# Optimization experiments

Hardware: AMD Instinct MI355X
Metric: run time of the kernel (lower is better)

The kernel has to match this reference:

```python
import jax, jax.numpy as jnp
import numpy as np

H = 128          # hidden_size
EF = 2           # expansion_factor
E = H * EF       # expanded hidden size
K = 4            # conv kernel size
R = 8            # dt_rank = ceil(128/16)
L = 2            # num_layers
BATCH = 2
SEQ = 1024
EPS = 1e-5


def rmsnorm(x, w):
    return x * jax.lax.rsqrt(jnp.mean(x * x, axis=-1, keepdims=True) + EPS) * w


def causal_conv1d(x, w, b):
    # x: (b, l, E); w: (E, 1, K) depthwise; left-pad K-1 => causal, output len l
    xt = jnp.transpose(x, (0, 2, 1))  # (b, E, l)
    out = jax.lax.conv_general_dilated(
        xt, w, window_strides=(1,), padding=[(K - 1, 0)],
        dimension_numbers=("NCH", "OIH", "NCH"), feature_group_count=E)
    out = out + b[None, :, None]
    return jnp.transpose(out, (0, 2, 1))


def sscan(xc, delta, A, Bm, Cm, Dp):
    # xc, delta: (b,l,E); A: (E,n); Bm, Cm: (b,l,n); Dp: (E,)
    deltaA = jnp.exp(jnp.einsum('bld,dn->bldn', delta, A))          # (b,l,E,n)
    deltaBx = jnp.einsum('bld,bln,bld->bldn', delta, Bm, xc)        # (b,l,E,n)

    def step(h, inp):
        dA_t, dBx_t, C_t = inp           # (b,E,n), (b,E,n), (b,n)
        h = dA_t * h + dBx_t
        y = jnp.einsum('bdn,bn->bd', h, C_t)
        return h, y

    b = xc.shape[0]
    h0 = jnp.zeros((b, E, A.shape[1]), dtype=xc.dtype)
    _, ys = jax.lax.scan(
        step, h0,
        (jnp.transpose(deltaA, (1, 0, 2, 3)),
         jnp.transpose(deltaBx, (1, 0, 2, 3)),
         jnp.transpose(Cm, (1, 0, 2))))
    y = jnp.transpose(ys, (1, 0, 2))     # (b,l,E)
    return y + Dp * xc


def mamba_block(x, in_w, in_b, out_w, out_b, pl_w, pl_b, dt_w, dt_b,
                conv_w, conv_b, A_log, Dp):
    xz = x @ in_w + in_b                 # (b,l,2E)
    xc, skip = jnp.split(xz, [E], axis=-1)
    xc = jax.nn.silu(causal_conv1d(xc, conv_w, conv_b))
    # ssm
    A = -jnp.exp(A_log)                  # (E,H)
    dbc = xc @ pl_w + pl_b               # (b,l,R+2H)
    delta, Bm, Cm = jnp.split(dbc, [R, R + H], axis=-1)
    delta = jax.nn.softplus(delta @ dt_w + dt_b)   # (b,l,E)
    y = sscan(xc, delta, A, Bm, Cm, Dp)
    y = y * jax.nn.silu(skip)
    return y @ out_w + out_b


def forward(x, in_w, in_b, out_w, out_b, pl_w, pl_b, dt_w, dt_b,
            conv_w, conv_b, A_log, Dp, norm_w, final_norm_w):
    for i in range(L):
        x = mamba_block(rmsnorm(x, norm_w[i]), in_w[i], in_b[i], out_w[i],
                        out_b[i], pl_w[i], pl_b[i], dt_w[i], dt_b[i],
                        conv_w[i], conv_b[i], A_log[i], Dp[i]) + x
    return rmsnorm(x, final_norm_w)


def setup_inputs() -> dict:
    key = jax.random.key(0)
    ks = jax.random.split(key, 12)
    s = 0.02
    x = jax.random.normal(ks[0], (BATCH, SEQ, H), dtype=jnp.float32)
    in_w = jax.random.normal(ks[1], (L, H, 2 * E)) * s
    in_b = jnp.zeros((L, 2 * E))
    out_w = jax.random.normal(ks[2], (L, E, H)) * s
    out_b = jnp.zeros((L, H))
    pl_w = jax.random.normal(ks[3], (L, E, R + 2 * H)) * s
    pl_b = jnp.zeros((L, R + 2 * H))
    dt_w = jax.random.normal(ks[4], (L, R, E)) * s
    dt_b = jnp.zeros((L, E))
    conv_w = jax.random.normal(ks[5], (L, E, 1, K)) * (1.0 / np.sqrt(K))
    conv_b = jnp.zeros((L, E))
    A_log = jnp.broadcast_to(jnp.log(jnp.arange(1, H + 1, dtype=jnp.float32)),
                             (L, E, H))
    Dp = jnp.ones((L, E))
    norm_w = jnp.ones((L, H))
    final_norm_w = jnp.ones((H,))
    return {"x": x, "in_w": in_w, "in_b": in_b, "out_w": out_w,
            "out_b": out_b, "pl_w": pl_w, "pl_b": pl_b, "dt_w": dt_w,
            "dt_b": dt_b, "conv_w": conv_w, "conv_b": conv_b,
            "A_log": A_log, "Dp": Dp, "norm_w": norm_w,
            "final_norm_w": final_norm_w}


def reference(x, in_w, in_b, out_w, out_b, pl_w, pl_b, dt_w, dt_b,
              conv_w, conv_b, A_log, Dp, norm_w, final_norm_w):
    return forward(x, in_w, in_b, out_w, out_b, pl_w, pl_b, dt_w, dt_b,
                   conv_w, conv_b, A_log, Dp, norm_w, final_norm_w)
```

## Files before the change

### kernel.cpp

```cpp
#include <hip/hip_runtime.h>
#include <hip/hip_bf16.h>

#define HH 128
#define EE 256
#define KK 4
#define RR 8
#define LL 2
#define BB 2
#define SS 1024
#define BT (BB*SS)
#define NJ (RR+2*HH)
#define GG 16
#define CH (SS/GG)
#define EPS 1e-5f
#define LOG2E 1.44269504088896f

__device__ __forceinline__ float silu_f(float v) {
    return v / (1.0f + __expf(-v));
}

__global__ __launch_bounds__(512) void k_norm_inproj(
    const float* __restrict__ xres, const float* __restrict__ inw,
    const float* __restrict__ inb, const float* __restrict__ nw,
    float* __restrict__ xz)
{
    __shared__ float xn[16][128];
    const int bt0 = blockIdx.x * 16;
    const int tid = threadIdx.x;
    {
        const int t = tid >> 5, g = tid & 31;
        const float4 xv = *(const float4*)(xres + (bt0 + t) * HH + g * 4);
        float ss = xv.x*xv.x + xv.y*xv.y + xv.z*xv.z + xv.w*xv.w;
        #pragma unroll
        for (int m = 16; m >= 1; m >>= 1) ss += __shfl_xor(ss, m);
        const float rs = rsqrtf(ss * (1.0f / HH) + EPS);
        const float4 wv = *(const float4*)(nw + g * 4);
        float4 o;
        o.x = xv.x * rs * wv.x; o.y = xv.y * rs * wv.y;
        o.z = xv.z * rs * wv.z; o.w = xv.w * rs * wv.w;
        *(float4*)(&xn[t][g * 4]) = o;
    }
    __syncthreads();
    const int j = tid;
    float acc[16];
    const float bj = inb[j];
    #pragma unroll
    for (int t = 0; t < 16; t++) acc[t] = bj;
    float w0n = inw[0*512 + j], w1n = inw[1*512 + j];
    float w2n = inw[2*512 + j], w3n = inw[3*512 + j];
    for (int k4 = 0; k4 < 32; k4++) {
        const float w0 = w0n, w1 = w1n, w2 = w2n, w3 = w3n;
        if (k4 < 31) {
            const int k = (k4 + 1) * 4;
            w0n = inw[(k+0)*512 + j]; w1n = inw[(k+1)*512 + j];
            w2n = inw[(k+2)*512 + j]; w3n = inw[(k+3)*512 + j];
        }
        const int k = k4 * 4;
        #pragma unroll
        for (int t = 0; t < 16; t++) {
            const float4 xv = *(const float4*)(&xn[t][k]);
            acc[t] += w0*xv.x + w1*xv.y + w2*xv.z + w3*xv.w;
        }
    }
    #pragma unroll
    for (int t = 0; t < 16; t++) xz[(bt0 + t) * 512 + j] = acc[t];
}

__global__ __launch_bounds__(256) void k_conv(
    const float* __restrict__ xz, const float* __restrict__ cw,
    const float* __restrict__ cb, float* __restrict__ xcT)
{
    const int e = threadIdx.x;
    const int tile = blockIdx.x;
    const int b = tile >> 6;
    const int t0 = (tile & 63) * 16;
    const float w0 = cw[e*4+0], w1 = cw[e*4+1], w2 = cw[e*4+2], w3 = cw[e*4+3];
    const float bias = cb[e];
    const float* xp = xz + (size_t)(b * SS) * 512 + e;
    float xm3 = (t0 >= 3) ? xp[(t0-3)*512] : 0.0f;
    float xm2 = (t0 >= 2) ? xp[(t0-2)*512] : 0.0f;
    float xm1 = (t0 >= 1) ? xp[(t0-1)*512] : 0.0f;
    float* orow = xcT + (size_t)e * BT + b * SS + t0;
    for (int jq = 0; jq < 4; jq++) {
        const int t = t0 + jq * 4;
        float4 ob; float v;
        const float x0 = xp[(t+0)*512];
        v = bias + w3*x0 + w2*xm1 + w1*xm2 + w0*xm3; ob.x = silu_f(v);
        const float x1 = xp[(t+1)*512];
        v = bias + w3*x1 + w2*x0 + w1*xm1 + w0*xm2;  ob.y = silu_f(v);
        const float x2 = xp[(t+2)*512];
        v = bias + w3*x2 + w2*x1 + w1*x0 + w0*xm1;   ob.z = silu_f(v);
        const float x3 = xp[(t+3)*512];
        v = bias + w3*x3 + w2*x2 + w1*x1 + w0*x0;    ob.w = silu_f(v);
        *(float4*)(orow + jq * 4) = ob;
        xm3 = x1; xm2 = x2; xm1 = x3;
    }
}

__global__ __launch_bounds__(320) void k_plproj(
    const float* __restrict__ xcT, const float* __restrict__ plw,
    const float* __restrict__ plb, float* __restrict__ dbcT)
{
    __shared__ float xs[8][256];
    const int bt0 = blockIdx.x * 8;
    const int tid = threadIdx.x;
    if (tid < 256) {
        const int e = tid;
        const float* p = xcT + (size_t)e * BT + bt0;
        const float4 a = *(const float4*)(p);
        const float4 c = *(const float4*)(p + 4);
        xs[0][e] = a.x; xs[1][e] = a.y; xs[2][e] = a.z; xs[3][e] = a.w;
        xs[4][e] = c.x; xs[5][e] = c.y; xs[6][e] = c.z; xs[7][e] = c.w;
    }
    __syncthreads();
    if (tid >= NJ) return;
    const int j = tid;
    float acc[8];
    const float bj = plb[j];
    #pragma unroll
    for (int t = 0; t < 8; t++) acc[t] = bj;
    float w0n = plw[0*NJ + j], w1n = plw[1*NJ + j];
    float w2n = plw[2*NJ + j], w3n = plw[3*NJ + j];
    for (int e4 = 0; e4 < 64; e4++) {
        const float w0 = w0n, w1 = w1n, w2 = w2n, w3 = w3n;
        if (e4 < 63) {
            const int e = (e4 + 1) * 4;
            w0n = plw[(e+0)*NJ + j]; w1n = plw[(e+1)*NJ + j];
            w2n = plw[(e+2)*NJ + j]; w3n = plw[(e+3)*NJ + j];
        }
        const int e = e4 * 4;
        #pragma unroll
        for (int t = 0; t < 8; t++) {
            const float4 xv = *(const float4*)(&xs[t][e]);
            acc[t] += w0*xv.x + w1*xv.y + w2*xv.z + w3*xv.w;
        }
    }
    float* orow = dbcT + (size_t)j * BT + bt0;
    *(float4*)(orow)     = make_float4(acc[0], acc[1], acc[2], acc[3]);
    *(float4*)(orow + 4) = make_float4(acc[4], acc[5], acc[6], acc[7]);
}

__global__ __launch_bounds__(256) void k_delta(
    const float* __restrict__ dbcT, const float* __restrict__ dtw,
    const float* __restrict__ dtb, const float* __restrict__ xcT,
    float* __restrict__ deltaT, float* __restrict__ sT)
{
    const int e = blockIdx.x >> 3;
    const int bt = (blockIdx.x & 7) * 256 + threadIdx.x;
    float d = dtb[e];
    #pragma unroll
    for (int r = 0; r < RR; r++) d += dtw[r*EE + e] * dbcT[(size_t)r * BT + bt];
    float sp;
    if (d > 15.0f) sp = d;
    else sp = log1pf(__expf(d));
    const float xc = xcT[(size_t)e * BT + bt];
    deltaT[(size_t)e * BT + bt] = sp;
    sT[(size_t)e * BT + bt] = sp * xc;
}

__global__ __launch_bounds__(128, 3) void k_scan_local(
    const float* __restrict__ dbcT, const float* __restrict__ deltaT,
    const float* __restrict__ sT, const float* __restrict__ Alog,
    float* __restrict__ yT, float* __restrict__ hchain,
    float* __restrict__ dsum)
{
    __shared__ float part[4][16][68];
    __shared__ float ybuf[4][CH];
    const int blk = blockIdx.x;
    const int wgid = (blk & 7) * 256 + (blk >> 3);
    const int eq = wgid & 63;
    const int r0 = wgid >> 6;
    const int b = r0 >> 4;
    const int g = r0 & 15;
    const int e0 = eq * 4;
    const int n = threadIdx.x;
    const int t0 = g * CH;

    float An[4], h[4], cum[4];
    #pragma unroll
    for (int ee = 0; ee < 4; ee++) {
        An[ee] = -__expf(Alog[(e0 + ee) * HH + n]) * LOG2E;
        h[ee] = 0.0f; cum[ee] = 0.0f;
    }
    const float* Brow = dbcT + (size_t)(RR + n) * BT + b * SS + t0;
    const float* Crow = dbcT + (size_t)(RR + HH + n) * BT + b * SS + t0;
    const float* dr[4]; const float* sr[4];
    #pragma unroll
    for (int ee = 0; ee < 4; ee++) {
        dr[ee] = deltaT + (size_t)(e0 + ee) * BT + b * SS + t0;
        sr[ee] = sT + (size_t)(e0 + ee) * BT + b * SS + t0;
    }
    float4 pB = *(const float4*)Brow;
    float4 pC = *(const float4*)Crow;
    float4 pd[4], ps[4];
    #pragma unroll
    for (int ee = 0; ee < 4; ee++) {
        pd[ee] = *(const float4*)dr[ee];
        ps[ee] = *(const float4*)sr[ee];
    }
    const int tl = n >> 3, jj = n & 7;
    for (int sc = 0; sc < 4; sc++) {
        #pragma unroll
        for (int q = 0; q < 4; q++) {
            const int qq = sc * 4 + q;
            const float4 cB = pB, cC = pC;
            float4 cd[4], cs[4];
            #pragma unroll
            for (int ee = 0; ee < 4; ee++) { cd[ee] = pd[ee]; cs[ee] = ps[ee]; }
            if (qq < 15) {
                const int t = (qq + 1) * 4;
                pB = *(const float4*)(Brow + t);
                pC = *(const float4*)(Crow + t);
                #pragma unroll
                for (int ee = 0; ee < 4; ee++) {
                    pd[ee] = *(const float4*)(dr[ee] + t);
                    ps[ee] = *(const float4*)(sr[ee] + t);
                }
            }
            #pragma unroll
            for (int ee = 0; ee < 4; ee++) {
                float a;
                a = exp2f(cd[ee].x * An[ee]); h[ee] = a*h[ee] + cs[ee].x*cB.x;
                part[ee][q*4+0][n] = h[ee] * cC.x;
                a = exp2f(cd[ee].y * An[ee]); h[ee] = a*h[ee] + cs[ee].y*cB.y;
                part[ee][q*4+1][n] = h[ee] * cC.y;
                a = exp2f(cd[ee].z * An[ee]); h[ee] = a*h[ee] + cs[ee].z*cB.z;
                part[ee][q*4+2][n] = h[ee] * cC.z;
                a = exp2f(cd[ee].w * An[ee]); h[ee] = a*h[ee] + cs[ee].w*cB.w;
                part[ee][q*4+3][n] = h[ee] * cC.w;
                cum[ee] += (cd[ee].x + cd[ee].y) + (cd[ee].z + cd[ee].w);
            }
        }
        __syncthreads();
        #pragma unroll
        for (int ee = 0; ee < 4; ee++) {
            float s0 = 0, s1 = 0, s2 = 0, s3 = 0;
            #pragma unroll
            for (int i = 0; i < 4; i++) {
                const float4 p = *(const float4*)(&part[ee][tl][jj*16 + i*4]);
                s0 += p.x; s1 += p.y; s2 += p.z; s3 += p.w;
            }
            float r = (s0 + s1) + (s2 + s3);
            r += __shfl_xor(r, 1); r += __shfl_xor(r, 2); r += __shfl_xor(r, 4);
            if (jj == 0) ybuf[ee][sc*16 + tl] = r;
        }
        __syncthreads();
    }
    {
        const int ee = n >> 5, tt = n & 31;
        float* yp = yT + (size_t)(e0 + ee) * BT + b * SS + t0;
        yp[tt] = ybuf[ee][tt];
        yp[tt + 32] = ybuf[ee][tt + 32];
    }
    #pragma unroll
    for (int ee = 0; ee < 4; ee++)
        hchain[(size_t)(((b * EE + e0 + ee) * GG) + g) * 128 + n] = h[ee];
    if (n == 0) {
        #pragma unroll
        for (int ee = 0; ee < 4; ee++)
            dsum[(b * EE + e0 + ee) * GG + g] = cum[ee];
    }
}

__global__ __launch_bounds__(128) void k_scan_combine(
    const float* __restrict__ Alog, const float* __restrict__ dsum,
    float* __restrict__ hchain)
{
    const int be = blockIdx.x;
    const int e = be & 255;
    const int n = threadIdx.x;
    const float An = -__expf(Alog[e * HH + n]) * LOG2E;
    float h = 0.0f;
    for (int g = 0; g < GG; g++) {
        float* p = hchain + (size_t)(be * GG + g) * 128 + n;
        const float he = *p;
        *p = h;
        const float ds = dsum[be * GG + g];
        h = exp2f(An * ds) * h + he;
    }
}

__global__ __launch_bounds__(128, 3) void k_scan_fix(
    const float* __restrict__ dbcT, const float* __restrict__ deltaT,
    const float* __restrict__ Alog, const float* __restrict__ hchain,
    float* __restrict__ yT)
{
    __shared__ float part[4][16][68];
    __shared__ float ybuf[4][CH];
    const int blk = blockIdx.x;
    const int wgid = (blk & 7) * 240 + (blk >> 3);
    const int eq = wgid & 63;
    const int r0 = wgid >> 6;
    const int b = r0 / 15;
    const int g = 1 + (r0 % 15);
    const int e0 = eq * 4;
    const int n = threadIdx.x;
    const int t0 = g * CH;

    float An[4], w[4], D[4];
    #pragma unroll
    for (int ee = 0; ee < 4; ee++) {
        An[ee] = -__expf(Alog[(e0 + ee) * HH + n]) * LOG2E;
        w[ee] = hchain[(size_t)(((b * EE + e0 + ee) * GG) + g) * 128 + n];
        D[ee] = 0.0f;
    }
    const float* Crow = dbcT + (size_t)(RR + HH + n) * BT + b * SS + t0;
    const float* dr[4];
    #pragma unroll
    for (int ee = 0; ee < 4; ee++)
        dr[ee] = deltaT + (size_t)(e0 + ee) * BT + b * SS + t0;

    float4 pC = *(const float4*)Crow;
    float4 pd[4];
    #pragma unroll
    for (int ee = 0; ee < 4; ee++) pd[ee] = *(const float4*)dr[ee];

    const int tl = n >> 3, jj = n & 7;
    for (int sc = 0; sc < 4; sc++) {
        #pragma unroll
        for (int q = 0; q < 4; q++) {
            const int qq = sc * 4 + q;
            const float4 cC = pC;
            float4 cd[4];
            #pragma unroll
            for (int ee = 0; ee < 4; ee++) cd[ee] = pd[ee];
            if (qq < 15) {
                const int t = (qq + 1) * 4;
                pC = *(const float4*)(Crow + t);
                #pragma unroll
                for (int ee = 0; ee < 4; ee++)
                    pd[ee] = *(const float4*)(dr[ee] + t);
            }
            #pragma unroll
            for (int ee = 0; ee < 4; ee++) {
                D[ee] += cd[ee].x; part[ee][q*4+0][n] = exp2f(An[ee]*D[ee]) * w[ee] * cC.x;
                D[ee] += cd[ee].y; part[ee][q*4+1][n] = exp2f(An[ee]*D[ee]) * w[ee] * cC.y;
                D[ee] += cd[ee].z; part[ee][q*4+2][n] = exp2f(An[ee]*D[ee]) * w[ee] * cC.z;
                D[ee] += cd[ee].w; part[ee][q*4+3][n] = exp2f(An[ee]*D[ee]) * w[ee] * cC.w;
            }
        }
        __syncthreads();
        #pragma unroll
        for (int ee = 0; ee < 4; ee++) {
            float s0 = 0, s1 = 0, s2 = 0, s3 = 0;
            #pragma unroll
            for (int i = 0; i < 4; i++) {
                const float4 p = *(const float4*)(&part[ee][tl][jj*16 + i*4]);
                s0 += p.x; s1 += p.y; s2 += p.z; s3 += p.w;
            }
            float r = (s0 + s1) + (s2 + s3);
            r += __shfl_xor(r, 1); r += __shfl_xor(r, 2); r += __shfl_xor(r, 4);
            if (jj == 0) ybuf[ee][sc*16 + tl] = r;
        }
        __syncthreads();
    }
    {
        const int ee = n >> 5, tt = n & 31;
        float* yp = yT + (size_t)(e0 + ee) * BT + b * SS + t0;
        yp[tt] += ybuf[ee][tt];
        yp[tt + 32] += ybuf[ee][tt + 32];
    }
}

__global__ __launch_bounds__(256) void k_gate_outproj(
    const float* __restrict__ yT, const float* __restrict__ xcT,
    const float* __restrict__ xz, const float* __restrict__ Dp,
    const float* __restrict__ ow, const float* __restrict__ ob,
    float* __restrict__ xres)
{
    __shared__ float gs[16][256];
    __shared__ float part2[16][128];
    const int bt0 = blockIdx.x * 16;
    const int tid = threadIdx.x;
    {
        const int e = tid;
        const float dp = Dp[e];
        const float* yp = yT + (size_t)e * BT + bt0;
        const float* xp = xcT + (size_t)e * BT + bt0;
        #pragma unroll
        for (int tq = 0; tq < 4; tq++) {
            const float4 y4 = *(const float4*)(yp + tq * 4);
            const float4 x4 = *(const float4*)(xp + tq * 4);
            float sk;
            sk = xz[(size_t)(bt0 + tq*4 + 0) * 512 + 256 + e];
            gs[tq*4+0][e] = (y4.x + dp * x4.x) * silu_f(sk);
            sk = xz[(size_t)(bt0 + tq*4 + 1) * 512 + 256 + e];
            gs[tq*4+1][e] = (y4.y + dp * x4.y) * silu_f(sk);
            sk = xz[(size_t)(bt0 + tq*4 + 2) * 512 + 256 + e];
            gs[tq*4+2][e] = (y4.z + dp * x4.z) * silu_f(sk);
            sk = xz[(size_t)(bt0 + tq*4 + 3) * 512 + 256 + e];
            gs[tq*4+3][e] = (y4.w + dp * x4.w) * silu_f(sk);
        }
    }
    __syncthreads();
    const int j = tid & 127;
    const int kh = tid >> 7;
    float acc[16];
    #pragma unroll
    for (int t = 0; t < 16; t++) acc[t] = 0.0f;
    const int eb = kh * 128;
    float w0n = ow[(eb+0)*HH + j], w1n = ow[(eb+1)*HH + j];
    float w2n = ow[(eb+2)*HH + j], w3n = ow[(eb+3)*HH + j];
    for (int e4 = 0; e4 < 32; e4++) {
        const float w0 = w0n, w1 = w1n, w2 = w2n, w3 = w3n;
        if (e4 < 31) {
            const int e = eb + (e4 + 1) * 4;
            w0n = ow[(e+0)*HH + j]; w1n = ow[(e+1)*HH + j];
            w2n = ow[(e+2)*HH + j]; w3n = ow[(e+3)*HH + j];
        }
        const int e = eb + e4 * 4;
        #pragma unroll
        for (int t = 0; t < 16; t++) {
            const float4 g4 = *(const float4*)(&gs[t][e]);
            acc[t] += w0*g4.x + w1*g4.y + w2*g4.z + w3*g4.w;
        }
    }
    if (kh == 1) {
        #pragma unroll
        for (int t = 0; t < 16; t++) part2[t][j] = acc[t];
    }
    __syncthreads();
    if (kh == 0) {
        const float bj = ob[j];
        #pragma unroll
        for (int t = 0; t < 16; t++) {
            const float r = acc[t] + part2[t][j] + bj
                          + xres[(size_t)(bt0 + t) * HH + j];
            xres[(size_t)(bt0 + t) * HH + j] = r;
        }
    }
}

__global__ __launch_bounds__(64) void k_finalnorm(
    const float* __restrict__ xres, const float* __restrict__ fw,
    float* __restrict__ out)
{
    const int bt = blockIdx.x;
    const int tid = threadIdx.x;
    const float2 v = *(const float2*)(xres + (size_t)bt * HH + tid * 2);
    float ss = v.x*v.x + v.y*v.y;
    #pragma unroll
    for (int m = 32; m >= 1; m >>= 1) ss += __shfl_xor(ss, m);
    const float rs = rsqrtf(ss * (1.0f / HH) + EPS);
    const float2 w = *(const float2*)(fw + tid * 2);
    float2 o; o.x = v.x * rs * w.x; o.y = v.y * rs * w.y;
    *(float2*)(out + (size_t)bt * HH + tid * 2) = o;
}

extern "C" void kernel_launch(void* const* d_in, const int* in_sizes, int n_in,
                              void* d_out, int out_size, void* d_ws, size_t ws_size,
                              hipStream_t stream)
{
    const float* x      = (const float*)d_in[0];
    const float* in_w   = (const float*)d_in[1];
    const float* in_b   = (const float*)d_in[2];
    const float* out_w  = (const float*)d_in[3];
    const float* out_b  = (const float*)d_in[4];
    const float* pl_w   = (const float*)d_in[5];
    const float* pl_b   = (const float*)d_in[6];
    const float* dt_w   = (const float*)d_in[7];
    const float* dt_b   = (const float*)d_in[8];
    const float* conv_w = (const float*)d_in[9];
    const float* conv_b = (const float*)d_in[10];
    const float* A_log  = (const float*)d_in[11];
    const float* Dp     = (const float*)d_in[12];
    const float* norm_w = (const float*)d_in[13];
    const float* fnw    = (const float*)d_in[14];

    float* ws     = (float*)d_ws;
    float* xres   = ws;
    float* xz     = xres   + 262144;
    float* xcT    = xz     + 1048576;
    float* dbcT   = xcT    + 524288;
    float* deltaT = dbcT   + 540672;
    float* sT     = deltaT + 524288;
    float* yT     = sT     + 524288;
    float* hchain = yT     + 524288;
    float* dsum   = hchain + 1048576;

    hipMemcpyAsync(xres, x, (size_t)262144 * sizeof(float),
                   hipMemcpyDeviceToDevice, stream);

    for (int l = 0; l < LL; l++) {
        k_norm_inproj<<<BT/16, 512, 0, stream>>>(
            xres, in_w + (size_t)l*HH*2*EE, in_b + (size_t)l*2*EE,
            norm_w + (size_t)l*HH, xz);
        k_conv<<<128, 256, 0, stream>>>(
            xz, conv_w + (size_t)l*EE*KK, conv_b + (size_t)l*EE, xcT);
        k_plproj<<<BT/8, 320, 0, stream>>>(
            xcT, pl_w + (size_t)l*EE*NJ, pl_b + (size_t)l*NJ, dbcT);
        k_delta<<<EE*8, 256, 0, stream>>>(
            dbcT, dt_w + (size_t)l*RR*EE, dt_b + (size_t)l*EE, xcT, deltaT, sT);
        k_scan_local<<<BB*GG*(EE/4), 128, 0, stream>>>(
            dbcT, deltaT, sT, A_log + (size_t)l*EE*HH, yT, hchain, dsum);
        k_scan_combine<<<BB*EE, 128, 0, stream>>>(
            A_log + (size_t)l*EE*HH, dsum, hchain);
        k_scan_fix<<<BB*(GG-1)*(EE/4), 128, 0, stream>>>(
            dbcT, deltaT, A_log + (size_t)l*EE*HH, hchain, yT);
        k_gate_outproj<<<BT/16, 256, 0, stream>>>(
            yT, xcT, xz, Dp + (size_t)l*EE,
            out_w + (size_t)l*EE*HH, out_b + (size_t)l*HH, xres);
    }
    k_finalnorm<<<BT, 64, 0, stream>>>(xres, fnw, (float*)d_out);
}
```

Before: 283.6 us.

## Interleave B/C into time-major layout, halve channels per scan block, move dsum to delta

The projection kernel now writes B and C into an interleaved layout with four timesteps grouped per state index, so each scan thread reads B and C for four steps with contiguous float4 loads. The chunk delta sums move into k_delta as a wave-level shuffle reduction, which removes the cumulative-sum work from the scan. The scan local and fix kernels now handle 2 channels per block instead of 4, doubling the grid and raising the occupancy hint to 4 blocks per CU. The intent is more parallelism and fewer registers per thread, at the cost of reloading B and C once per 2 channels instead of once per 4.

```diff
diff --git a/kernel.cpp b/kernel.cpp
--- a/kernel.cpp
+++ b/kernel.cpp
@@ -99,7 +99,8 @@
 
 __global__ __launch_bounds__(320) void k_plproj(
     const float* __restrict__ xcT, const float* __restrict__ plw,
-    const float* __restrict__ plb, float* __restrict__ dbcT)
+    const float* __restrict__ plb, float* __restrict__ dtrows,
+    float* __restrict__ BC4)
 {
     __shared__ float xs[8][256];
     const int bt0 = blockIdx.x * 8;
@@ -135,105 +136,107 @@
             acc[t] += w0*xv.x + w1*xv.y + w2*xv.z + w3*xv.w;
         }
     }
-    float* orow = dbcT + (size_t)j * BT + bt0;
-    *(float4*)(orow)     = make_float4(acc[0], acc[1], acc[2], acc[3]);
-    *(float4*)(orow + 4) = make_float4(acc[4], acc[5], acc[6], acc[7]);
+    if (j < RR) {
+        float* orow = dtrows + (size_t)j * BT + bt0;
+        *(float4*)(orow)     = make_float4(acc[0], acc[1], acc[2], acc[3]);
+        *(float4*)(orow + 4) = make_float4(acc[4], acc[5], acc[6], acc[7]);
+    } else {
+        const int isC = (j >= RR + HH);
+        const int nn = isC ? (j - RR - HH) : (j - RR);
+        const int tq0 = bt0 >> 2;
+        float* p0 = BC4 + ((size_t)tq0 * 128 + nn) * 8 + (isC ? 4 : 0);
+        *(float4*)p0 = make_float4(acc[0], acc[1], acc[2], acc[3]);
+        float* p1 = BC4 + ((size_t)(tq0 + 1) * 128 + nn) * 8 + (isC ? 4 : 0);
+        *(float4*)p1 = make_float4(acc[4], acc[5], acc[6], acc[7]);
+    }
 }
 
 __global__ __launch_bounds__(256) void k_delta(
-    const float* __restrict__ dbcT, const float* __restrict__ dtw,
+    const float* __restrict__ dtrows, const float* __restrict__ dtw,
     const float* __restrict__ dtb, const float* __restrict__ xcT,
-    float* __restrict__ deltaT, float* __restrict__ sT)
+    float* __restrict__ deltaT, float* __restrict__ sT,
+    float* __restrict__ dsum)
 {
     const int e = blockIdx.x >> 3;
     const int bt = (blockIdx.x & 7) * 256 + threadIdx.x;
     float d = dtb[e];
     #pragma unroll
-    for (int r = 0; r < RR; r++) d += dtw[r*EE + e] * dbcT[(size_t)r * BT + bt];
+    for (int r = 0; r < RR; r++) d += dtw[r*EE + e] * dtrows[(size_t)r * BT + bt];
     float sp;
     if (d > 15.0f) sp = d;
     else sp = log1pf(__expf(d));
     const float xc = xcT[(size_t)e * BT + bt];
     deltaT[(size_t)e * BT + bt] = sp;
     sT[(size_t)e * BT + bt] = sp * xc;
-}
-
-__global__ __launch_bounds__(128, 3) void k_scan_local(
-    const float* __restrict__ dbcT, const float* __restrict__ deltaT,
+    float cs = sp;
+    #pragma unroll
+    for (int m = 1; m <= 32; m <<= 1) cs += __shfl_xor(cs, m);
+    if ((threadIdx.x & 63) == 0) {
+        const int b = bt >> 10;
+        const int g = (bt & 1023) >> 6;
+        dsum[(b * EE + e) * GG + g] = cs;
+    }
+}
+
+__global__ __launch_bounds__(128, 4) void k_scan_local(
+    const float* __restrict__ BC4, const float* __restrict__ deltaT,
     const float* __restrict__ sT, const float* __restrict__ Alog,
-    float* __restrict__ yT, float* __restrict__ hchain,
-    float* __restrict__ dsum)
-{
-    __shared__ float part[4][16][68];
-    __shared__ float ybuf[4][CH];
+    float* __restrict__ yT, float* __restrict__ hchain)
+{
+    __shared__ float part[2][16][68];
+    __shared__ float ybuf[2][CH];
     const int blk = blockIdx.x;
-    const int wgid = (blk & 7) * 256 + (blk >> 3);
-    const int eq = wgid & 63;
-    const int r0 = wgid >> 6;
+    const int wgid = (blk & 7) * 512 + (blk >> 3);
+    const int eq = wgid & 127;
+    const int r0 = wgid >> 7;
     const int b = r0 >> 4;
     const int g = r0 & 15;
-    const int e0 = eq * 4;
+    const int e0 = eq * 2;
     const int n = threadIdx.x;
     const int t0 = g * CH;
 
-    float An[4], h[4], cum[4];
-    #pragma unroll
-    for (int ee = 0; ee < 4; ee++) {
-        An[ee] = -__expf(Alog[(e0 + ee) * HH + n]) * LOG2E;
-        h[ee] = 0.0f; cum[ee] = 0.0f;
-    }
-    const float* Brow = dbcT + (size_t)(RR + n) * BT + b * SS + t0;
-    const float* Crow = dbcT + (size_t)(RR + HH + n) * BT + b * SS + t0;
-    const float* dr[4]; const float* sr[4];
-    #pragma unroll
-    for (int ee = 0; ee < 4; ee++) {
-        dr[ee] = deltaT + (size_t)(e0 + ee) * BT + b * SS + t0;
-        sr[ee] = sT + (size_t)(e0 + ee) * BT + b * SS + t0;
-    }
-    float4 pB = *(const float4*)Brow;
-    float4 pC = *(const float4*)Crow;
-    float4 pd[4], ps[4];
-    #pragma unroll
-    for (int ee = 0; ee < 4; ee++) {
-        pd[ee] = *(const float4*)dr[ee];
-        ps[ee] = *(const float4*)sr[ee];
-    }
+    float An0 = -__expf(Alog[(e0+0) * HH + n]) * LOG2E;
+    float An1 = -__expf(Alog[(e0+1) * HH + n]) * LOG2E;
+    float h0 = 0.0f, h1 = 0.0f;
+    const float* bc = BC4 + ((size_t)((b * 256 + g * 16) * 128 + n)) * 8;
+    const float* dr0 = deltaT + (size_t)(e0+0) * BT + b * SS + t0;
+    const float* dr1 = deltaT + (size_t)(e0+1) * BT + b * SS + t0;
+    const float* sr0 = sT + (size_t)(e0+0) * BT + b * SS + t0;
+    const float* sr1 = sT + (size_t)(e0+1) * BT + b * SS + t0;
+
+    float4 pB = *(const float4*)(bc);
+    float4 pC = *(const float4*)(bc + 4);
+    float4 pd0 = *(const float4*)dr0, pd1 = *(const float4*)dr1;
+    float4 ps0 = *(const float4*)sr0, ps1 = *(const float4*)sr1;
+
     const int tl = n >> 3, jj = n & 7;
     for (int sc = 0; sc < 4; sc++) {
         #pragma unroll
         for (int q = 0; q < 4; q++) {
             const int qq = sc * 4 + q;
             const float4 cB = pB, cC = pC;
-            float4 cd[4], cs[4];
-            #pragma unroll
-            for (int ee = 0; ee < 4; ee++) { cd[ee] = pd[ee]; cs[ee] = ps[ee]; }
+            const float4 cd0 = pd0, cd1 = pd1, cs0 = ps0, cs1 = ps1;
             if (qq < 15) {
+                const size_t off = (size_t)(qq + 1) * 1024;
+                pB = *(const float4*)(bc + off);
+                pC = *(const float4*)(bc + off + 4);
                 const int t = (qq + 1) * 4;
-                pB = *(const float4*)(Brow + t);
-                pC = *(const float4*)(Crow + t);
-                #pragma unroll
-                for (int ee = 0; ee < 4; ee++) {
-                    pd[ee] = *(const float4*)(dr[ee] + t);
-                    ps[ee] = *(const float4*)(sr[ee] + t);
-                }
+                pd0 = *(const float4*)(dr0 + t); pd1 = *(const float4*)(dr1 + t);
+                ps0 = *(const float4*)(sr0 + t); ps1 = *(const float4*)(sr1 + t);
             }
-            #pragma unroll
-            for (int ee = 0; ee < 4; ee++) {
-                float a;
-                a = exp2f(cd[ee].x * An[ee]); h[ee] = a*h[ee] + cs[ee].x*cB.x;
-                part[ee][q*4+0][n] = h[ee] * cC.x;
-                a = exp2f(cd[ee].y * An[ee]); h[ee] = a*h[ee] + cs[ee].y*cB.y;
-                part[ee][q*4+1][n] = h[ee] * cC.y;
-                a = exp2f(cd[ee].z * An[ee]); h[ee] = a*h[ee] + cs[ee].z*cB.z;
-                part[ee][q*4+2][n] = h[ee] * cC.z;
-                a = exp2f(cd[ee].w * An[ee]); h[ee] = a*h[ee] + cs[ee].w*cB.w;
-                part[ee][q*4+3][n] = h[ee] * cC.w;
-                cum[ee] += (cd[ee].x + cd[ee].y) + (cd[ee].z + cd[ee].w);
-            }
+            float a;
+            a = exp2f(cd0.x*An0); h0 = a*h0 + cs0.x*cB.x; part[0][q*4+0][n] = h0*cC.x;
+            a = exp2f(cd0.y*An0); h0 = a*h0 + cs0.y*cB.y; part[0][q*4+1][n] = h0*cC.y;
+            a = exp2f(cd0.z*An0); h0 = a*h0 + cs0.z*cB.z; part[0][q*4+2][n] = h0*cC.z;
+            a = exp2f(cd0.w*An0); h0 = a*h0 + cs0.w*cB.w; part[0][q*4+3][n] = h0*cC.w;
+            a = exp2f(cd1.x*An1); h1 = a*h1 + cs1.x*cB.x; part[1][q*4+0][n] = h1*cC.x;
+            a = exp2f(cd1.y*An1); h1 = a*h1 + cs1.y*cB.y; part[1][q*4+1][n] = h1*cC.y;
+            a = exp2f(cd1.z*An1); h1 = a*h1 + cs1.z*cB.z; part[1][q*4+2][n] = h1*cC.z;
+            a = exp2f(cd1.w*An1); h1 = a*h1 + cs1.w*cB.w; part[1][q*4+3][n] = h1*cC.w;
         }
         __syncthreads();
         #pragma unroll
-        for (int ee = 0; ee < 4; ee++) {
+        for (int ee = 0; ee < 2; ee++) {
             float s0 = 0, s1 = 0, s2 = 0, s3 = 0;
             #pragma unroll
             for (int i = 0; i < 4; i++) {
@@ -247,19 +250,11 @@
         __syncthreads();
     }
     {
-        const int ee = n >> 5, tt = n & 31;
-        float* yp = yT + (size_t)(e0 + ee) * BT + b * SS + t0;
-        yp[tt] = ybuf[ee][tt];
-        yp[tt + 32] = ybuf[ee][tt + 32];
-    }
-    #pragma unroll
-    for (int ee = 0; ee < 4; ee++)
-        hchain[(size_t)(((b * EE + e0 + ee) * GG) + g) * 128 + n] = h[ee];
-    if (n == 0) {
-        #pragma unroll
-        for (int ee = 0; ee < 4; ee++)
-            dsum[(b * EE + e0 + ee) * GG + g] = cum[ee];
-    }
+        const int ee = n >> 6, tt = n & 63;
+        yT[(size_t)(e0 + ee) * BT + b * SS + t0 + tt] = ybuf[ee][tt];
+    }
+    hchain[(size_t)(((b * EE + e0 + 0) * GG) + g) * 128 + n] = h0;
+    hchain[(size_t)(((b * EE + e0 + 1) * GG) + g) * 128 + n] = h1;
 }
 
 __global__ __launch_bounds__(128) void k_scan_combine(
@@ -280,40 +275,34 @@
     }
 }
 
-__global__ __launch_bounds__(128, 3) void k_scan_fix(
-    const float* __restrict__ dbcT, const float* __restrict__ deltaT,
+__global__ __launch_bounds__(128, 4) void k_scan_fix(
+    const float* __restrict__ BC4, const float* __restrict__ deltaT,
     const float* __restrict__ Alog, const float* __restrict__ hchain,
     float* __restrict__ yT)
 {
-    __shared__ float part[4][16][68];
-    __shared__ float ybuf[4][CH];
+    __shared__ float part[2][16][68];
+    __shared__ float ybuf[2][CH];
     const int blk = blockIdx.x;
-    const int wgid = (blk & 7) * 240 + (blk >> 3);
-    const int eq = wgid & 63;
-    const int r0 = wgid >> 6;
+    const int wgid = (blk & 7) * 480 + (blk >> 3);
+    const int eq = wgid & 127;
+    const int r0 = wgid >> 7;
     const int b = r0 / 15;
     const int g = 1 + (r0 % 15);
-    const int e0 = eq * 4;
+    const int e0 = eq * 2;
     const int n = threadIdx.x;
     const int t0 = g * CH;
 
-    float An[4], w[4], D[4];
-    #pragma unroll
-    for (int ee = 0; ee < 4; ee++) {
-        An[ee] = -__expf(Alog[(e0 + ee) * HH + n]) * LOG2E;
-        w[ee] = hchain[(size_t)(((b * EE + e0 + ee) * GG) + g) * 128 + n];
-        D[ee] = 0.0f;
-    }
-    const float* Crow = dbcT + (size_t)(RR + HH + n) * BT + b * SS + t0;
-    const float* dr[4];
-    #pragma unroll
-    for (int ee = 0; ee < 4; ee++)
-        dr[ee] = deltaT + (size_t)(e0 + ee) * BT + b * SS + t0;
-
-    float4 pC = *(const float4*)Crow;
-    float4 pd[4];
-    #pragma unroll
-    for (int ee = 0; ee < 4; ee++) pd[ee] = *(const float4*)dr[ee];
+    const float An0 = -__expf(Alog[(e0+0) * HH + n]) * LOG2E;
+    const float An1 = -__expf(Alog[(e0+1) * HH + n]) * LOG2E;
+    const float w0 = hchain[(size_t)(((b * EE + e0 + 0) * GG) + g) * 128 + n];
+    const float w1 = hchain[(size_t)(((b * EE + e0 + 1) * GG) + g) * 128 + n];
+    float D0 = 0.0f, D1 = 0.0f;
+    const float* bc = BC4 + ((size_t)((b * 256 + g * 16) * 128 + n)) * 8;
+    const float* dr0 = deltaT + (size_t)(e0+0) * BT + b * SS + t0;
+    const float* dr1 = deltaT + (size_t)(e0+1) * BT + b * SS + t0;
+
+    float4 pC = *(const float4*)(bc + 4);
+    float4 pd0 = *(const float4*)dr0, pd1 = *(const float4*)dr1;
 
     const int tl = n >> 3, jj = n & 7;
     for (int sc = 0; sc < 4; sc++) {
@@ -321,27 +310,25 @@
         for (int q = 0; q < 4; q++) {
             const int qq = sc * 4 + q;
             const float4 cC = pC;
-            float4 cd[4];
-            #pragma unroll
-            for (int ee = 0; ee < 4; ee++) cd[ee] = pd[ee];
+            const float4 cd0 = pd0, cd1 = pd1;
             if (qq < 15) {
+                const size_t off = (size_t)(qq + 1) * 1024;
+                pC = *(const float4*)(bc + off + 4);
                 const int t = (qq + 1) * 4;
-                pC = *(const float4*)(Crow + t);
-                #pragma unroll
-                for (int ee = 0; ee < 4; ee++)
-                    pd[ee] = *(const float4*)(dr[ee] + t);
+                pd0 = *(const float4*)(dr0 + t); pd1 = *(const float4*)(dr1 + t);
             }
-            #pragma unroll
-            for (int ee = 0; ee < 4; ee++) {
-                D[ee] += cd[ee].x; part[ee][q*4+0][n] = exp2f(An[ee]*D[ee]) * w[ee] * cC.x;
-                D[ee] += cd[ee].y; part[ee][q*4+1][n] = exp2f(An[ee]*D[ee]) * w[ee] * cC.y;
-                D[ee] += cd[ee].z; part[ee][q*4+2][n] = exp2f(An[ee]*D[ee]) * w[ee] * cC.z;
-                D[ee] += cd[ee].w; part[ee][q*4+3][n] = exp2f(An[ee]*D[ee]) * w[ee] * cC.w;
-            }
+            D0 += cd0.x; part[0][q*4+0][n] = exp2f(An0*D0) * w0 * cC.x;
+            D0 += cd0.y; part[0][q*4+1][n] = exp2f(An0*D0) * w0 * cC.y;
+            D0 += cd0.z; part[0][q*4+2][n] = exp2f(An0*D0) * w0 * cC.z;
+            D0 += cd0.w; part[0][q*4+3][n] = exp2f(An0*D0) * w0 * cC.w;
+            D1 += cd1.x; part[1][q*4+0][n] = exp2f(An1*D1) * w1 * cC.x;
+            D1 += cd1.y; part[1][q*4+1][n] = exp2f(An1*D1) * w1 * cC.y;
+            D1 += cd1.z; part[1][q*4+2][n] = exp2f(An1*D1) * w1 * cC.z;
+            D1 += cd1.w; part[1][q*4+3][n] = exp2f(An1*D1) * w1 * cC.w;
         }
         __syncthreads();
         #pragma unroll
-        for (int ee = 0; ee < 4; ee++) {
+        for (int ee = 0; ee < 2; ee++) {
             float s0 = 0, s1 = 0, s2 = 0, s3 = 0;
             #pragma unroll
             for (int i = 0; i < 4; i++) {
@@ -355,10 +342,8 @@
         __syncthreads();
     }
     {
-        const int ee = n >> 5, tt = n & 31;
-        float* yp = yT + (size_t)(e0 + ee) * BT + b * SS + t0;
-        yp[tt] += ybuf[ee][tt];
-        yp[tt + 32] += ybuf[ee][tt + 32];
+        const int ee = n >> 6, tt = n & 63;
+        yT[(size_t)(e0 + ee) * BT + b * SS + t0 + tt] += ybuf[ee][tt];
     }
 }
 
@@ -471,8 +456,9 @@
     float* xres   = ws;
     float* xz     = xres   + 262144;
     float* xcT    = xz     + 1048576;
-    float* dbcT   = xcT    + 524288;
-    float* deltaT = dbcT   + 540672;
+    float* dtrows = xcT    + 524288;
+    float* BC4    = dtrows + 16384;
+    float* deltaT = BC4    + 524288;
     float* sT     = deltaT + 524288;
     float* yT     = sT     + 524288;
     float* hchain = yT     + 524288;
@@ -488,15 +474,16 @@
         k_conv<<<128, 256, 0, stream>>>(
             xz, conv_w + (size_t)l*EE*KK, conv_b + (size_t)l*EE, xcT);
         k_plproj<<<BT/8, 320, 0, stream>>>(
-            xcT, pl_w + (size_t)l*EE*NJ, pl_b + (size_t)l*NJ, dbcT);
+            xcT, pl_w + (size_t)l*EE*NJ, pl_b + (size_t)l*NJ, dtrows, BC4);
         k_delta<<<EE*8, 256, 0, stream>>>(
-            dbcT, dt_w + (size_t)l*RR*EE, dt_b + (size_t)l*EE, xcT, deltaT, sT);
-        k_scan_local<<<BB*GG*(EE/4), 128, 0, stream>>>(
-            dbcT, deltaT, sT, A_log + (size_t)l*EE*HH, yT, hchain, dsum);
+            dtrows, dt_w + (size_t)l*RR*EE, dt_b + (size_t)l*EE, xcT,
+            deltaT, sT, dsum);
+        k_scan_local<<<BB*GG*(EE/2), 128, 0, stream>>>(
+            BC4, deltaT, sT, A_log + (size_t)l*EE*HH, yT, hchain);
         k_scan_combine<<<BB*EE, 128, 0, stream>>>(
             A_log + (size_t)l*EE*HH, dsum, hchain);
-        k_scan_fix<<<BB*(GG-1)*(EE/4), 128, 0, stream>>>(
-            dbcT, deltaT, A_log + (size_t)l*EE*HH, hchain, yT);
+        k_scan_fix<<<BB*(GG-1)*(EE/2), 128, 0, stream>>>(
+            BC4, deltaT, A_log + (size_t)l*EE*HH, hchain, yT);
         k_gate_outproj<<<BT/16, 256, 0, stream>>>(
             yT, xcT, xz, Dp + (size_t)l*EE,
             out_w + (size_t)l*EE*HH, out_b + (size_t)l*HH, xres);
```

Result: faster. 248.7 us (-12.3%).
